# Kernel tuning notes

Measured on AMD Instinct MI355X. Metric: run time of the kernel, lower is better.

The kernel has to match this reference:

```python
import jax, jax.numpy as jnp
import numpy as np

N, E, IN, H, OUT = 50000, 800000, 256, 128, 64


def setup_inputs() -> dict:
    key = jax.random.key(0)
    ks = jax.random.split(key, 4)
    x = jax.random.normal(ks[0], (N, IN), dtype=jnp.float32)
    edge_index = jax.random.randint(ks[1], (2, E), 0, N, dtype=jnp.int64)
    W1 = jax.random.normal(ks[2], (IN, H), dtype=jnp.float32) / np.float32(np.sqrt(IN))
    b1 = jnp.zeros((H,), jnp.float32)
    W2 = jax.random.normal(ks[3], (H, OUT), dtype=jnp.float32) / np.float32(np.sqrt(H))
    b2 = jnp.zeros((OUT,), jnp.float32)
    return {"x": x, "edge_index": edge_index, "W1": W1, "b1": b1, "W2": W2, "b2": b2}


def _gcn_conv(x, W, b, src, dst, norm, n):
    # PyG GCNConv: linear transform, then symmetric-normalized aggregation, then bias
    h = x @ W                                        # [n, d_out]
    agg = jax.ops.segment_sum(h[src] * norm[:, None], dst, num_segments=n)
    return agg + b


def reference(x, edge_index, W1, b1, W2, b2):
    n = x.shape[0]
    loop = jnp.arange(n, dtype=edge_index.dtype)
    # add self-loops (GCNConv default add_self_loops=True)
    src = jnp.concatenate([edge_index[0], loop])
    dst = jnp.concatenate([edge_index[1], loop])
    # symmetric normalization deg^{-1/2} A_hat deg^{-1/2}
    deg = jax.ops.segment_sum(jnp.ones(src.shape, jnp.float32), dst, num_segments=n)
    dinv = jnp.where(deg > 0, jax.lax.rsqrt(deg), 0.0)
    norm = dinv[src] * dinv[dst]                     # [E + n]
    h = jax.nn.relu(_gcn_conv(x, W1, b1, src, dst, norm, n))
    return _gcn_conv(h, W2, b2, src, dst, norm, n)
```

## Files before the change

### kernel.cpp

```cpp
#include <hip/hip_runtime.h>


#define DI 256
#define DH 128
#define DO 64

typedef unsigned short ushort;
typedef unsigned int uint;
using bf16x8 = __attribute__((ext_vector_type(8))) short;
using f32x4  = __attribute__((ext_vector_type(4))) float;

__device__ __forceinline__ ushort f2b(float f) {
    union { float f; uint u; } v; v.f = f;
    uint r = (v.u + 0x7fffu + ((v.u >> 16) & 1u)) >> 16;
    return (ushort)r;
}
__device__ __forceinline__ float blo(uint v) { return __uint_as_float(v << 16); }
__device__ __forceinline__ float bhi(uint v) { return __uint_as_float(v & 0xffff0000u); }

__global__ void deg_count(const int* __restrict__ dst, int* __restrict__ deg, int E) {
    int e = blockIdx.x * blockDim.x + threadIdx.x;
    if (e < E) atomicAdd(&deg[dst[e]], 1);
}

__global__ void scan1(const int* __restrict__ deg, int* __restrict__ off,
                      int* __restrict__ bsum, int n) {
    __shared__ int sh[256];
    int i = blockIdx.x * 256 + threadIdx.x;
    int v = (i < n) ? deg[i] : 0;
    sh[threadIdx.x] = v;
    __syncthreads();
    for (int o = 1; o < 256; o <<= 1) {
        int t = (threadIdx.x >= o) ? sh[threadIdx.x - o] : 0;
        __syncthreads();
        sh[threadIdx.x] += t;
        __syncthreads();
    }
    if (i < n) off[i] = sh[threadIdx.x] - v;
    if (threadIdx.x == 255) bsum[blockIdx.x] = sh[255];
}

__global__ void scan2(int* __restrict__ bsum, int nb) {
    __shared__ int sh[256];
    int v = (threadIdx.x < nb) ? bsum[threadIdx.x] : 0;
    sh[threadIdx.x] = v;
    __syncthreads();
    for (int o = 1; o < 256; o <<= 1) {
        int t = (threadIdx.x >= o) ? sh[threadIdx.x - o] : 0;
        __syncthreads();
        sh[threadIdx.x] += t;
        __syncthreads();
    }
    bsum[threadIdx.x] = sh[threadIdx.x] - v;
}

__global__ void scan3(int* __restrict__ off, const int* __restrict__ bsum,
                      int* __restrict__ cursor, int n, int E) {
    int i = blockIdx.x * 256 + threadIdx.x;
    if (i < n) {
        int o = off[i] + bsum[blockIdx.x];
        off[i] = o;
        cursor[i] = o;
    }
    if (i == 0) off[n] = E;
}

__global__ void make_dinv(const int* __restrict__ deg, float* __restrict__ dinv, int n) {
    int i = blockIdx.x * blockDim.x + threadIdx.x;
    if (i < n) dinv[i] = rsqrtf((float)deg[i] + 1.0f);
}

__global__ void fill_csr(const int* __restrict__ src, const int* __restrict__ dst,
                         int* __restrict__ cursor, int* __restrict__ csr, int E) {
    int e = blockIdx.x * blockDim.x + threadIdx.x;
    if (e < E) {
        int p = atomicAdd(&cursor[dst[e]], 1);
        csr[p] = src[e];
    }
}

__global__ void wt_cvt(const float* __restrict__ W, ushort* __restrict__ Wt, int K, int M) {
    int idx = blockIdx.x * 256 + threadIdx.x;
    if (idx < K * M) {
        int m = idx / K, k = idx % K;
        Wt[idx] = f2b(W[(long)k * M + m]);
    }
}

template<int K, int M, bool INF32>
__global__ __launch_bounds__(256) void mfma_gemm(const void* __restrict__ Xv,
                                                 const ushort* __restrict__ Wt,
                                                 const float* __restrict__ dinv,
                                                 ushort* __restrict__ Y, int n) {
    constexpr int ROWB = K * 2;
    constexpr int CT = M / 64;
    __shared__ ushort Xs[64 * K];
    const int t = threadIdx.x;
    const int r0 = blockIdx.x * 64;

    {
        const int row = t & 63, c = t >> 6;
        const int gr = r0 + row;
        if (INF32) {
            const float4* Xr = (const float4*)((const float*)Xv + (long)gr * K);
#pragma unroll
            for (int j = 0; j < K / 32; ++j) {
                float4 a, b;
                if (gr < n) {
                    a = Xr[c * (K / 16) + 2 * j];
                    b = Xr[c * (K / 16) + 2 * j + 1];
                } else {
                    a = make_float4(0.f, 0.f, 0.f, 0.f); b = a;
                }
                ushort u[8] = {f2b(a.x), f2b(a.y), f2b(a.z), f2b(a.w),
                               f2b(b.x), f2b(b.y), f2b(b.z), f2b(b.w)};
                int byte = row * ROWB + c * (K / 2) + j * 16;
                byte ^= (row & 7) << 4;
                *(uint4*)((char*)Xs + byte) = *(const uint4*)u;
            }
        } else {
            const uint4* Xr = (const uint4*)((const ushort*)Xv + (long)gr * K);
#pragma unroll
            for (int j = 0; j < K / 32; ++j) {
                uint4 v = make_uint4(0u, 0u, 0u, 0u);
                if (gr < n) v = Xr[c * (K / 32) + j];
                int byte = row * ROWB + c * (K / 2) + j * 16;
                byte ^= (row & 7) << 4;
                *(uint4*)((char*)Xs + byte) = v;
            }
        }
    }
    __syncthreads();

    const int w  = t >> 6;
    const int l  = t & 63;
    const int lr = l & 15;
    const int lg = l >> 4;
    f32x4 acc[4][CT] = {};

#pragma unroll
    for (int ks = 0; ks < K / 32; ++ks) {
        bf16x8 bfr[CT];
#pragma unroll
        for (int ct = 0; ct < CT; ++ct) {
            int col = w * (M / 4) + ct * 16 + lr;
            bfr[ct] = *(const bf16x8*)&Wt[(long)col * K + ks * 32 + lg * 8];
        }
        bf16x8 afr[4];
#pragma unroll
        for (int rt = 0; rt < 4; ++rt) {
            int row = rt * 16 + lr;
            int byte = row * ROWB + ks * 64 + lg * 16;
            byte ^= (row & 7) << 4;
            afr[rt] = *(const bf16x8*)((const char*)Xs + byte);
        }
#pragma unroll
        for (int rt = 0; rt < 4; ++rt)
#pragma unroll
            for (int ct = 0; ct < CT; ++ct)
                acc[rt][ct] = __builtin_amdgcn_mfma_f32_16x16x32_bf16(
                    afr[rt], bfr[ct], acc[rt][ct], 0, 0, 0);
    }

#pragma unroll
    for (int rt = 0; rt < 4; ++rt)
#pragma unroll
        for (int i = 0; i < 4; ++i) {
            int gr2 = r0 + rt * 16 + lg * 4 + i;
            if (gr2 < n) {
                float dv = dinv[gr2];
#pragma unroll
                for (int ct = 0; ct < CT; ++ct) {
                    int col = w * (M / 4) + ct * 16 + lr;
                    Y[(long)gr2 * M + col] = f2b(dv * acc[rt][ct][i]);
                }
            }
        }
}

template<int M, bool RELU, bool OUTF32>
__global__ void gather_fin(const int* __restrict__ off, const int* __restrict__ csr,
                           const ushort* __restrict__ Hs, const float* __restrict__ dinv,
                           const float* __restrict__ b, void* __restrict__ Yv, int n) {
    constexpr int G = M / 8;
    constexpr int NPB = 256 / G;
    int g = threadIdx.x / G;
    int j = threadIdx.x % G;
    int i = blockIdx.x * NPB + g;
    if (i >= n) return;
    const uint4* H4 = (const uint4*)Hs;
    float acc[8];
    {
        uint4 s = H4[(long)i * G + j];
        acc[0] = blo(s.x); acc[1] = bhi(s.x);
        acc[2] = blo(s.y); acc[3] = bhi(s.y);
        acc[4] = blo(s.z); acc[5] = bhi(s.z);
        acc[6] = blo(s.w); acc[7] = bhi(s.w);
    }
    int k = off[i], ke = off[i + 1];
    for (; k + 3 < ke; k += 4) {
        int s0 = csr[k], s1 = csr[k + 1], s2 = csr[k + 2], s3 = csr[k + 3];
        uint4 a0 = H4[(long)s0 * G + j];
        uint4 a1 = H4[(long)s1 * G + j];
        uint4 a2 = H4[(long)s2 * G + j];
        uint4 a3 = H4[(long)s3 * G + j];
        acc[0] += blo(a0.x) + blo(a1.x) + blo(a2.x) + blo(a3.x);
        acc[1] += bhi(a0.x) + bhi(a1.x) + bhi(a2.x) + bhi(a3.x);
        acc[2] += blo(a0.y) + blo(a1.y) + blo(a2.y) + blo(a3.y);
        acc[3] += bhi(a0.y) + bhi(a1.y) + bhi(a2.y) + bhi(a3.y);
        acc[4] += blo(a0.z) + blo(a1.z) + blo(a2.z) + blo(a3.z);
        acc[5] += bhi(a0.z) + bhi(a1.z) + bhi(a2.z) + bhi(a3.z);
        acc[6] += blo(a0.w) + blo(a1.w) + blo(a2.w) + blo(a3.w);
        acc[7] += bhi(a0.w) + bhi(a1.w) + bhi(a2.w) + bhi(a3.w);
    }
    for (; k < ke; ++k) {
        uint4 a = H4[(long)csr[k] * G + j];
        acc[0] += blo(a.x); acc[1] += bhi(a.x);
        acc[2] += blo(a.y); acc[3] += bhi(a.y);
        acc[4] += blo(a.z); acc[5] += bhi(a.z);
        acc[6] += blo(a.w); acc[7] += bhi(a.w);
    }
    float di = dinv[i];
    float4 b0 = ((const float4*)b)[j * 2];
    float4 b1 = ((const float4*)b)[j * 2 + 1];
    float r[8];
    r[0] = di * acc[0] + b0.x; r[1] = di * acc[1] + b0.y;
    r[2] = di * acc[2] + b0.z; r[3] = di * acc[3] + b0.w;
    r[4] = di * acc[4] + b1.x; r[5] = di * acc[5] + b1.y;
    r[6] = di * acc[6] + b1.z; r[7] = di * acc[7] + b1.w;
    if (RELU) {
#pragma unroll
        for (int m = 0; m < 8; ++m) r[m] = fmaxf(r[m], 0.f);
    }
    if (OUTF32) {
        float* Y = (float*)Yv;
        *(float4*)&Y[(long)i * M + j * 8]     = make_float4(r[0], r[1], r[2], r[3]);
        *(float4*)&Y[(long)i * M + j * 8 + 4] = make_float4(r[4], r[5], r[6], r[7]);
    } else {
        ushort* Y = (ushort*)Yv;
        uint4 o;
        o.x = (uint)f2b(r[0]) | ((uint)f2b(r[1]) << 16);
        o.y = (uint)f2b(r[2]) | ((uint)f2b(r[3]) << 16);
        o.z = (uint)f2b(r[4]) | ((uint)f2b(r[5]) << 16);
        o.w = (uint)f2b(r[6]) | ((uint)f2b(r[7]) << 16);
        *(uint4*)&Y[(long)i * M + j * 8] = o;
    }
}

extern "C" void kernel_launch(void* const* d_in, const int* in_sizes, int n_in,
                              void* d_out, int out_size, void* d_ws, size_t ws_size,
                              hipStream_t stream) {
    const float* x  = (const float*)d_in[0];
    const int*   ei = (const int*)d_in[1];
    const float* W1 = (const float*)d_in[2];
    const float* b1 = (const float*)d_in[3];
    const float* W2 = (const float*)d_in[4];
    const float* b2 = (const float*)d_in[5];
    float* out = (float*)d_out;

    const int n = in_sizes[0] / DI;
    const int E = in_sizes[1] / 2;
    const int* src = ei;
    const int* dst = ei + E;
    const int nb = (n + 255) / 256;
    const int np = nb * 256;

    int*    deg    = (int*)d_ws;
    float*  dinv   = (float*)d_ws;
    int*    off    = deg + np;
    int*    cursor = off + np + 256;
    int*    bsum   = cursor + np;
    int*    csr    = bsum + 256;
    ushort* w1t    = (ushort*)(csr + E);
    ushort* w2t    = w1t + DH * DI;
    ushort* h0s    = w2t + DO * DH;
    ushort* h      = h0s + (size_t)n * DH;
    ushort* h1s    = h0s;

    const int eb = (E + 255) / 256;

    hipMemsetAsync(deg, 0, (size_t)n * 4, stream);
    deg_count<<<eb, 256, 0, stream>>>(dst, deg, E);
    scan1<<<nb, 256, 0, stream>>>(deg, off, bsum, n);
    scan2<<<1, 256, 0, stream>>>(bsum, nb);
    scan3<<<nb, 256, 0, stream>>>(off, bsum, cursor, n, E);
    make_dinv<<<nb, 256, 0, stream>>>(deg, dinv, n);
    fill_csr<<<eb, 256, 0, stream>>>(src, dst, cursor, csr, E);
    wt_cvt<<<(DI * DH + 255) / 256, 256, 0, stream>>>(W1, w1t, DI, DH);
    wt_cvt<<<(DH * DO + 255) / 256, 256, 0, stream>>>(W2, w2t, DH, DO);

    const int gblk = (n + 63) / 64;
    mfma_gemm<DI, DH, true><<<gblk, 256, 0, stream>>>(x, w1t, dinv, h0s, n);
    gather_fin<DH, true, false><<<(n + 15) / 16, 256, 0, stream>>>(off, csr, h0s, dinv, b1, h, n);
    mfma_gemm<DH, DO, false><<<gblk, 256, 0, stream>>>(h, w2t, dinv, h1s, n);
    gather_fin<DO, false, true><<<(n + 31) / 32, 256, 0, stream>>>(off, csr, h1s, dinv, b2, out, n);
}
```

Before: 269.1 us.

## Build CSR via fixed-capacity 64-node buckets sorted locally in LDS

Replaces the per-node degree count, three-kernel prefix scan, dinv kernel and atomic CSR fill with three kernels. The first scatters packed (src, local dst) pairs into fixed-capacity buckets of 64 destination nodes. The second is a single-block scan over bucket counts. The third loads each bucket into LDS, builds a local histogram, writes offsets and dinv, and places the edges. This cuts kernel launches and moves the per-node atomics into shared memory. In exchange, every edge does a global atomic on one of only about 800 bucket counters, which adds contention. Any bucket holding more than 4096 edges silently drops edges, and the single-block scan caps the bucket count at 1024.

```diff
diff --git a/kernel.cpp b/kernel.cpp
--- a/kernel.cpp
+++ b/kernel.cpp
@@ -4,6 +4,7 @@
 #define DI 256
 #define DH 128
 #define DO 64
+#define CAP 4096
 
 typedef unsigned short ushort;
 typedef unsigned int uint;
@@ -18,64 +19,78 @@
 __device__ __forceinline__ float blo(uint v) { return __uint_as_float(v << 16); }
 __device__ __forceinline__ float bhi(uint v) { return __uint_as_float(v & 0xffff0000u); }
 
-__global__ void deg_count(const int* __restrict__ dst, int* __restrict__ deg, int E) {
-    int e = blockIdx.x * blockDim.x + threadIdx.x;
-    if (e < E) atomicAdd(&deg[dst[e]], 1);
-}
-
-__global__ void scan1(const int* __restrict__ deg, int* __restrict__ off,
-                      int* __restrict__ bsum, int n) {
-    __shared__ int sh[256];
-    int i = blockIdx.x * 256 + threadIdx.x;
-    int v = (i < n) ? deg[i] : 0;
-    sh[threadIdx.x] = v;
+__global__ void scatter_pairs(const int* __restrict__ src, const int* __restrict__ dst,
+                              int* __restrict__ cur, uint* __restrict__ pairs, int E) {
+    int e = blockIdx.x * 256 + threadIdx.x;
+    if (e >= E) return;
+    int s = src[e], d = dst[e];
+    int b = d >> 6;
+    int p = atomicAdd(&cur[b], 1);
+    if (p < CAP) pairs[((long)b << 12) + p] = ((uint)s << 6) | (uint)(d & 63);
+}
+
+__global__ void scanB(const int* __restrict__ cur, int* __restrict__ boff,
+                      int* __restrict__ off, int nbk, int n, int E) {
+    __shared__ int tsum[256];
+    int v[4];
+    int base = threadIdx.x * 4;
+    int s = 0;
+#pragma unroll
+    for (int j = 0; j < 4; ++j) {
+        v[j] = (base + j < nbk) ? min(cur[base + j], CAP) : 0;
+        s += v[j];
+    }
+    tsum[threadIdx.x] = s;
     __syncthreads();
     for (int o = 1; o < 256; o <<= 1) {
-        int t = (threadIdx.x >= o) ? sh[threadIdx.x - o] : 0;
+        int t = (threadIdx.x >= o) ? tsum[threadIdx.x - o] : 0;
         __syncthreads();
-        sh[threadIdx.x] += t;
+        tsum[threadIdx.x] += t;
         __syncthreads();
     }
-    if (i < n) off[i] = sh[threadIdx.x] - v;
-    if (threadIdx.x == 255) bsum[blockIdx.x] = sh[255];
-}
-
-__global__ void scan2(int* __restrict__ bsum, int nb) {
-    __shared__ int sh[256];
-    int v = (threadIdx.x < nb) ? bsum[threadIdx.x] : 0;
-    sh[threadIdx.x] = v;
-    __syncthreads();
-    for (int o = 1; o < 256; o <<= 1) {
-        int t = (threadIdx.x >= o) ? sh[threadIdx.x - o] : 0;
-        __syncthreads();
-        sh[threadIdx.x] += t;
-        __syncthreads();
-    }
-    bsum[threadIdx.x] = sh[threadIdx.x] - v;
-}
-
-__global__ void scan3(int* __restrict__ off, const int* __restrict__ bsum,
-                      int* __restrict__ cursor, int n, int E) {
-    int i = blockIdx.x * 256 + threadIdx.x;
-    if (i < n) {
-        int o = off[i] + bsum[blockIdx.x];
-        off[i] = o;
-        cursor[i] = o;
-    }
-    if (i == 0) off[n] = E;
-}
-
-__global__ void make_dinv(const int* __restrict__ deg, float* __restrict__ dinv, int n) {
-    int i = blockIdx.x * blockDim.x + threadIdx.x;
-    if (i < n) dinv[i] = rsqrtf((float)deg[i] + 1.0f);
-}
-
-__global__ void fill_csr(const int* __restrict__ src, const int* __restrict__ dst,
-                         int* __restrict__ cursor, int* __restrict__ csr, int E) {
-    int e = blockIdx.x * blockDim.x + threadIdx.x;
-    if (e < E) {
-        int p = atomicAdd(&cursor[dst[e]], 1);
-        csr[p] = src[e];
+    int run = tsum[threadIdx.x] - s;
+#pragma unroll
+    for (int j = 0; j < 4; ++j) {
+        if (base + j < nbk) boff[base + j] = run;
+        run += v[j];
+    }
+    if (threadIdx.x == 0) off[n] = E;
+}
+
+__global__ __launch_bounds__(256) void bucket_csr(const int* __restrict__ cur,
+                                                  const int* __restrict__ boff,
+                                                  const uint* __restrict__ pairs,
+                                                  int* __restrict__ off,
+                                                  float* __restrict__ dinv,
+                                                  int* __restrict__ csr, int n) {
+    __shared__ uint eL[CAP];
+    __shared__ int lh[64], lo[64], lc[64];
+    const int b = blockIdx.x;
+    const int cnt = min(cur[b], CAP);
+    const int bo = boff[b];
+    for (int i = threadIdx.x; i < cnt; i += 256) eL[i] = pairs[((long)b << 12) + i];
+    if (threadIdx.x < 64) lh[threadIdx.x] = 0;
+    __syncthreads();
+    for (int i = threadIdx.x; i < cnt; i += 256) atomicAdd(&lh[eL[i] & 63], 1);
+    __syncthreads();
+    if (threadIdx.x == 0) {
+        int r = 0;
+        for (int l = 0; l < 64; ++l) { lo[l] = r; r += lh[l]; }
+    }
+    __syncthreads();
+    int node = b * 64 + threadIdx.x;
+    if (threadIdx.x < 64) {
+        if (node < n) {
+            off[node]  = bo + lo[threadIdx.x];
+            dinv[node] = rsqrtf((float)lh[threadIdx.x] + 1.0f);
+        }
+        lc[threadIdx.x] = lo[threadIdx.x];
+    }
+    __syncthreads();
+    for (int i = threadIdx.x; i < cnt; i += 256) {
+        uint v = eL[i];
+        int slot = atomicAdd(&lc[v & 63], 1);
+        csr[bo + slot] = (int)(v >> 6);
     }
 }
 
@@ -262,30 +277,26 @@
     const int E = in_sizes[1] / 2;
     const int* src = ei;
     const int* dst = ei + E;
-    const int nb = (n + 255) / 256;
-    const int np = nb * 256;
-
-    int*    deg    = (int*)d_ws;
-    float*  dinv   = (float*)d_ws;
-    int*    off    = deg + np;
-    int*    cursor = off + np + 256;
-    int*    bsum   = cursor + np;
-    int*    csr    = bsum + 256;
-    ushort* w1t    = (ushort*)(csr + E);
-    ushort* w2t    = w1t + DH * DI;
-    ushort* h0s    = w2t + DO * DH;
-    ushort* h      = h0s + (size_t)n * DH;
-    ushort* h1s    = h0s;
-
-    const int eb = (E + 255) / 256;
-
-    hipMemsetAsync(deg, 0, (size_t)n * 4, stream);
-    deg_count<<<eb, 256, 0, stream>>>(dst, deg, E);
-    scan1<<<nb, 256, 0, stream>>>(deg, off, bsum, n);
-    scan2<<<1, 256, 0, stream>>>(bsum, nb);
-    scan3<<<nb, 256, 0, stream>>>(off, bsum, cursor, n, E);
-    make_dinv<<<nb, 256, 0, stream>>>(deg, dinv, n);
-    fill_csr<<<eb, 256, 0, stream>>>(src, dst, cursor, csr, E);
+    const int nbk = (n + 63) / 64;
+    const int np  = ((n + 255) / 256) * 256;
+
+    int*    cur  = (int*)d_ws;
+    int*    boff = cur + 1024;
+    int*    off  = boff + 1024;
+    float*  dinv = (float*)(off + np + 256);
+    int*    csr  = (int*)(dinv + np);
+    ushort* w1t  = (ushort*)(csr + E);
+    ushort* w2t  = w1t + DH * DI;
+    ushort* h0s  = w2t + DO * DH;
+    ushort* h    = h0s + (size_t)n * DH;
+    uint*   pairs = (uint*)(h + (size_t)n * DH);
+    ushort* h1s  = h0s;
+
+    hipMemsetAsync(cur, 0, 1024 * 4, stream);
+    scatter_pairs<<<(E + 255) / 256, 256, 0, stream>>>(src, dst, cur, pairs, E);
+    scanB<<<1, 256, 0, stream>>>(cur, boff, off, nbk, n, E);
+    bucket_csr<<<nbk, 256, 0, stream>>>(cur, boff, pairs, off, dinv, csr, n);
+
     wt_cvt<<<(DI * DH + 255) / 256, 256, 0, stream>>>(W1, w1t, DI, DH);
     wt_cvt<<<(DH * DO + 255) / 256, 256, 0, stream>>>(W2, w2t, DH, DO);
 
```

Result: slower. 385.6 us (+43.3%).
